# Kernel optimization log

Measured on AMD Instinct MI355X. Metric: run time of the kernel, lower is better.

## Reference

```python
import jax, jax.numpy as jnp
import numpy as np

B_, N, C = 1024, 64, 512
H = 16          # num_heads
NW = 64         # number of windows (B_ % NW == 0)


def setup_inputs() -> dict:
    key = jax.random.key(0)
    ks = jax.random.split(key, 7)
    return {
        "x": jax.random.normal(ks[0], (B_, N, C), jnp.float32),
        "mask": jax.random.normal(ks[1], (NW, N, N), jnp.float32),
        "qkv_w": jax.random.normal(ks[2], (C, 3 * C), jnp.float32) * 0.02,
        "qkv_b": jax.random.normal(ks[3], (3 * C,), jnp.float32) * 0.02,
        "proj_w": jax.random.normal(ks[4], (C, C), jnp.float32) * 0.02,
        "proj_b": jax.random.normal(ks[5], (C,), jnp.float32) * 0.02,
        "bias_table": jax.random.normal(ks[6], (2 * N - 1, H), jnp.float32) * 0.02,
    }


def reference(x, mask, qkv_w, qkv_b, proj_w, proj_b, bias_table):
    b_, n, c = x.shape
    h = bias_table.shape[1]
    ws = (bias_table.shape[0] + 1) // 2  # window_size, == n here
    d = c // h
    scale = d ** -0.5

    qkv = x @ qkv_w + qkv_b                                   # [B_, N, 3C]
    qkv = qkv.reshape(b_, n, 3, h, d).transpose(2, 0, 3, 1, 4)  # [3, B_, H, N, d]
    q, k, v = qkv[0] * scale, qkv[1], qkv[2]

    attn = jnp.einsum('bhnd,bhmd->bhnm', q, k)                # [B_, H, N, N]

    coords = jnp.arange(ws)
    rel_idx = coords[:, None] - coords[None, :] + ws - 1       # [ws, ws]
    bias = bias_table[rel_idx].transpose(2, 0, 1)              # [H, ws, ws]
    attn = attn + bias[None]

    nw = mask.shape[0]
    attn = attn.reshape(b_ // nw, nw, h, n, n) + mask[None, :, None]
    attn = attn.reshape(-1, h, n, n)
    attn = jax.nn.softmax(attn, axis=-1)

    out = jnp.einsum('bhnm,bhmd->bhnd', attn, v)               # [B_, H, N, d]
    # Faithful to the TF code: v keeps a leading singleton dim after tf.split,
    # so attn@v is [1, B_, H, N, d]; perm [0,2,1,3,4] swaps B_ and H before
    # the final reshape to (B_, N, C).
    out = out[None].transpose(0, 2, 1, 3, 4).reshape(b_, n, c)
    return out @ proj_w + proj_b
```

## Files before the change

kernel.cpp:

```cpp
#include <hip/hip_runtime.h>
#include <hip/hip_bf16.h>
#include <stdint.h>

typedef __attribute__((ext_vector_type(4))) float f32x4;
typedef __attribute__((ext_vector_type(8))) short s16x8;

__device__ __forceinline__ short f2bf(float f) {
  union { float f; uint32_t u; } v; v.f = f;
  uint32_t r = v.u + 0x7FFFu + ((v.u >> 16) & 1u);
  return (short)(r >> 16);
}
__device__ __forceinline__ uint32_t pack2bf(float a, float b) {
  return (uint32_t)(uint16_t)f2bf(a) | ((uint32_t)(uint16_t)f2bf(b) << 16);
}

__device__ __forceinline__ void async16(const void* g, void* l) {
  __builtin_amdgcn_global_load_lds(
      (const __attribute__((address_space(1))) void*)g,
      (__attribute__((address_space(3))) void*)l, 16, 0, 0);
}

__global__ __launch_bounds__(256) void k_cast_bf16(const float* __restrict__ in,
                                                   short* __restrict__ out, int n8) {
  int i = blockIdx.x * 256 + threadIdx.x;
  if (i >= n8) return;
  const float4* p = (const float4*)in + (size_t)i * 2;
  float4 a = p[0], b = p[1];
  s16x8 o;
  o[0] = f2bf(a.x); o[1] = f2bf(a.y); o[2] = f2bf(a.z); o[3] = f2bf(a.w);
  o[4] = f2bf(b.x); o[5] = f2bf(b.y); o[6] = f2bf(b.z); o[7] = f2bf(b.w);
  ((s16x8*)out)[i] = o;
}

__global__ __launch_bounds__(256) void k_transpose_cast(const float* __restrict__ in,
                                                        short* __restrict__ out,
                                                        int K, int N) {
  __shared__ float tile[64][65];
  const int bx = blockIdx.x;
  const int by = blockIdx.y;
  const int tx = threadIdx.x & 63, ty = threadIdx.x >> 6;
#pragma unroll
  for (int r = ty; r < 64; r += 4)
    tile[r][tx] = in[(size_t)(by * 64 + r) * N + bx * 64 + tx];
  __syncthreads();
#pragma unroll
  for (int r = ty; r < 64; r += 4)
    out[(size_t)(bx * 64 + r) * K + by * 64 + tx] = f2bf(tile[tx][r]);
}

#define TILE_SH 16384

template <int OUTMODE, int NBN, int KK>
__global__ __launch_bounds__(512, 2) void k_gemm256p(const short* __restrict__ A,
                                                     const short* __restrict__ Bw,
                                                     const float* __restrict__ bias,
                                                     void* __restrict__ C,
                                                     int N, int nrounds) {
  __shared__ short lds[2 * 2 * TILE_SH];
  const int t = threadIdx.x;
  const int w = t >> 6, l = t & 63;
  const int wm = w >> 2, wn = w & 3;
  const int swz = (((int)blockIdx.x & 7) << 5) + ((int)blockIdx.x >> 3);

  const int NT = KK >> 6;
  const int NS = nrounds * NT;

  auto stage = [&](const short* __restrict__ G, int row0, int kt, short* dst) {
#pragma unroll
    for (int L = 0; L < 2; ++L) {
      int cw = L * 512 + (t & ~63);
      int c = cw + l;
      int r = c >> 3, s = c & 7;
      async16(G + (size_t)(row0 + r) * KK + kt + ((s ^ (r & 7)) << 3), dst + cw * 8);
    }
  };
  auto issueA = [&](int step, int bmv, int hf) {
    int kt = step & 7;
    stage(A, bmv * 256 + hf * 128, kt * 64, lds + (kt & 1) * 32768 + hf * 8192);
  };
  auto issueB = [&](int step, int bnv, int hf) {
    int kt = step & 7;
    stage(Bw, bnv * 256 + hf * 128, kt * 64, lds + (kt & 1) * 32768 + TILE_SH + hf * 8192);
  };

  const int g = l >> 4, v = l & 7;
  int ofsA[2], ofsB[2];
#pragma unroll
  for (int ks = 0; ks < 2; ++ks) {
    ofsA[ks] = (wm * 128 + (l & 15)) * 64 + (((ks * 4 + g) ^ v) << 3);
    ofsB[ks] = (wn * 64 + (l & 15)) * 64 + (((ks * 4 + g) ^ v) << 3);
  }

  f32x4 acc[8][4] = {};
  s16x8 bfr[4][2];

  {
    const int bm0 = swz / NBN, bn0 = swz % NBN;
    issueB(0, bn0, 0); issueB(0, bn0, 1);
    issueA(0, bm0, 0); issueA(0, bm0, 1);
    issueB(1, bn0, 0); issueB(1, bn0, 1);
  }
  asm volatile("s_waitcnt vmcnt(4)" ::: "memory");
  __builtin_amdgcn_s_barrier();

#define PHASE(AI0, STAGE_STMT, TAIL_STMT)                                                                      \
  {                                                                                                            \
    s16x8 a00 = *(const s16x8*)(Ab + ofsA[0] + (AI0) * 1024);                                                  \
    s16x8 a01 = *(const s16x8*)(Ab + ofsA[1] + (AI0) * 1024);                                                  \
    s16x8 a10 = *(const s16x8*)(Ab + ofsA[0] + ((AI0) + 1) * 1024);                                            \
    s16x8 a11 = *(const s16x8*)(Ab + ofsA[1] + ((AI0) + 1) * 1024);                                            \
    STAGE_STMT;                                                                                                \
    __builtin_amdgcn_s_barrier();                                                                              \
    asm volatile("s_waitcnt lgkmcnt(0)" ::: "memory");                                                         \
    __builtin_amdgcn_s_setprio(1);                                                                             \
    _Pragma("unroll")                                                                                          \
    for (int nj = 0; nj < 4; ++nj) {                                                                           \
      acc[(AI0)][nj] = __builtin_amdgcn_mfma_f32_16x16x32_bf16(a00, bfr[nj][0], acc[(AI0)][nj], 0, 0, 0);      \
      acc[(AI0)][nj] = __builtin_amdgcn_mfma_f32_16x16x32_bf16(a01, bfr[nj][1], acc[(AI0)][nj], 0, 0, 0);      \
      acc[(AI0) + 1][nj] = __builtin_amdgcn_mfma_f32_16x16x32_bf16(a10, bfr[nj][0], acc[(AI0) + 1][nj], 0, 0, 0); \
      acc[(AI0) + 1][nj] = __builtin_amdgcn_mfma_f32_16x16x32_bf16(a11, bfr[nj][1], acc[(AI0) + 1][nj], 0, 0, 0); \
    }                                                                                                          \
    __builtin_amdgcn_s_setprio(0);                                                                             \
    TAIL_STMT;                                                                                                 \
    __builtin_amdgcn_s_barrier();                                                                              \
  }

  for (int j = 0; j < nrounds; ++j) {
    const int tauc = swz + (j << 8);
    const int bmc = tauc / NBN, bnc = tauc % NBN;
    for (int T = 0; T < NT; ++T) {
      const int s = (j << 3) + T;
      const int s1 = s + 1, s2 = s + 2;
      const int tau1 = swz + (((s1) >> 3) << 8);
      const int tau2 = swz + (((s2) >> 3) << 8);
      const int bm1 = tau1 / NBN;
      const int bn2 = tau2 % NBN;
      const short* Ab = lds + (T & 1) * 32768;
      const short* Bb = Ab + TILE_SH;
#pragma unroll
      for (int nj = 0; nj < 4; ++nj)
#pragma unroll
        for (int ks = 0; ks < 2; ++ks)
          bfr[nj][ks] = *(const s16x8*)(Bb + ofsB[ks] + nj * 1024);

      PHASE(0, if (s1 < NS) issueA(s1, bm1, 0), );
      PHASE(2, if (s1 < NS) issueA(s1, bm1, 1), );
      PHASE(4, if (s2 < NS) issueB(s2, bn2, 0), );
      PHASE(6, if (s2 < NS) issueB(s2, bn2, 1),
            if (s2 < NS) { asm volatile("s_waitcnt vmcnt(4)" ::: "memory"); }
            else if (s1 < NS) { asm volatile("s_waitcnt vmcnt(0)" ::: "memory"); });
    }

#pragma unroll
    for (int ai = 0; ai < 8; ++ai)
#pragma unroll
      for (int nj = 0; nj < 4; ++nj) {
        int col = bnc * 256 + wn * 64 + nj * 16 + (l & 15);
        float bv = bias[col];
#pragma unroll
        for (int r = 0; r < 4; ++r) {
          int row = bmc * 256 + wm * 128 + ai * 16 + (l >> 4) * 4 + r;
          float vv = acc[ai][nj][r] + bv;
          if (OUTMODE == 1) {
            ((float*)C)[(size_t)row * N + col] = vv;
          } else if (OUTMODE == 0) {
            ((short*)C)[(size_t)row * N + col] = f2bf(vv);
          } else {
            int bb = row >> 6, nn = row & 63;
            int sel = col >> 9, hh = (col >> 5) & 15, dd = col & 31;
            ((short*)C)[(((size_t)(bb * 48 + hh * 3 + sel)) << 11) + (nn << 5) + dd] = f2bf(vv);
          }
        }
      }
#pragma unroll
    for (int ai = 0; ai < 8; ++ai)
#pragma unroll
      for (int nj = 0; nj < 4; ++nj)
        acc[ai][nj] = (f32x4){0.f, 0.f, 0.f, 0.f};
  }
#undef PHASE
}

__global__ __launch_bounds__(256) void k_attn(const short* __restrict__ qkv2,
                                              const float* __restrict__ mask,
                                              const float* __restrict__ bias_table,
                                              short* __restrict__ Y) {
  __shared__ float mask_lds[64 * 64];
  __shared__ float bias_lds[4][128];
  __shared__ short p_lds[4][64][72];
  __shared__ short v_lds[4][64][40];

  const int t = threadIdx.x, wv = t >> 6, ln = t & 63;
  const int b = blockIdx.x;
  const int h = blockIdx.y * 4 + wv;
  const int hi = ln >> 4, lo = ln & 15;

  const float4* mk = (const float4*)(mask + (size_t)(b & 63) * 4096);
#pragma unroll
  for (int u = 0; u < 4; ++u) {
    int idx = t + 256 * u;
    int row = idx >> 4, c4 = (idx & 15) * 4;
    *(float4*)&mask_lds[row * 64 + (c4 ^ ((row & 7) << 2))] = mk[idx];
  }
  for (int u = ln; u < 127; u += 64) bias_lds[wv][u] = bias_table[u * 16 + h];

  const short* base = qkv2 + ((size_t)(b * 16 + h)) * 3 * 2048;
  const short* vg = base + 4096;
#pragma unroll
  for (int u = 0; u < 4; ++u) {
    int row = u * 16 + (ln >> 2), c8 = (ln & 3) * 8;
    *(s16x8*)&v_lds[wv][row][c8] = *(const s16x8*)(vg + row * 32 + c8);
  }
  __syncthreads();

  s16x8 qf[4], kf[4];
#pragma unroll
  for (int i = 0; i < 4; ++i) {
    qf[i] = *(const s16x8*)(base + (16 * i + lo) * 32 + hi * 8);
    kf[i] = *(const s16x8*)(base + 2048 + (16 * i + lo) * 32 + hi * 8);
  }
  f32x4 s2[4][4] = {};
#pragma unroll
  for (int j = 0; j < 4; ++j)
#pragma unroll
    for (int i = 0; i < 4; ++i)
      s2[j][i] = __builtin_amdgcn_mfma_f32_16x16x32_bf16(kf[j], qf[i], s2[j][i], 0, 0, 0);

  const float scale = 0.17677669529663687f;
#pragma unroll
  for (int i = 0; i < 4; ++i) {
    const int n = 16 * i + lo;
    const int msw = (n & 7) << 2;
    float x[16];
    float vmax = -1e30f;
#pragma unroll
    for (int j = 0; j < 4; ++j)
#pragma unroll
      for (int r = 0; r < 4; ++r) {
        int m = 16 * j + 4 * hi + r;
        float xx = s2[j][i][r] * scale + bias_lds[wv][n - m + 63] +
                   mask_lds[n * 64 + (m ^ msw)];
        x[j * 4 + r] = xx;
        vmax = fmaxf(vmax, xx);
      }
    vmax = fmaxf(vmax, __shfl_xor(vmax, 16, 64));
    vmax = fmaxf(vmax, __shfl_xor(vmax, 32, 64));
    float sum = 0.f;
#pragma unroll
    for (int u = 0; u < 16; ++u) {
      x[u] = __expf(x[u] - vmax);
      sum += x[u];
    }
    sum += __shfl_xor(sum, 16, 64);
    sum += __shfl_xor(sum, 32, 64);
    float rsv = 1.0f / sum;
#pragma unroll
    for (int j = 0; j < 4; ++j)
#pragma unroll
      for (int rp = 0; rp < 2; ++rp)
        *(uint32_t*)&p_lds[wv][n][16 * j + 4 * hi + rp * 2] =
            pack2bf(x[j * 4 + rp * 2] * rsv, x[j * 4 + rp * 2 + 1] * rsv);
  }

  f32x4 o2[2][4] = {};
#pragma unroll
  for (int kk = 0; kk < 2; ++kk) {
    s16x8 pa[4];
#pragma unroll
    for (int i2 = 0; i2 < 4; ++i2)
      pa[i2] = *(const s16x8*)&p_lds[wv][16 * i2 + lo][kk * 32 + hi * 8];
#pragma unroll
    for (int j2 = 0; j2 < 2; ++j2) {
      s16x8 vf;
#pragma unroll
      for (int jj = 0; jj < 8; ++jj)
        vf[jj] = v_lds[wv][kk * 32 + hi * 8 + jj][16 * j2 + lo];
#pragma unroll
      for (int i2 = 0; i2 < 4; ++i2)
        o2[j2][i2] = __builtin_amdgcn_mfma_f32_16x16x32_bf16(vf, pa[i2], o2[j2][i2], 0, 0, 0);
    }
  }

  const int rr = h * 64 + (b >> 4);
#pragma unroll
  for (int i2 = 0; i2 < 4; ++i2) {
    int ss = (b & 15) * 4 + i2;
    short* yr = Y + ((size_t)rr * 64 + ss) * 512 + lo * 32 + 4 * hi;
#pragma unroll
    for (int j2 = 0; j2 < 2; ++j2) {
      uint2 pk;
      pk.x = pack2bf(o2[j2][i2][0], o2[j2][i2][1]);
      pk.y = pack2bf(o2[j2][i2][2], o2[j2][i2][3]);
      *(uint2*)(yr + 16 * j2) = pk;
    }
  }
}

extern "C" void kernel_launch(void* const* d_in, const int* in_sizes, int n_in,
                              void* d_out, int out_size, void* d_ws, size_t ws_size,
                              hipStream_t stream) {
  const float* x      = (const float*)d_in[0];
  const float* mask   = (const float*)d_in[1];
  const float* qkv_w  = (const float*)d_in[2];
  const float* qkv_b  = (const float*)d_in[3];
  const float* proj_w = (const float*)d_in[4];
  const float* proj_b = (const float*)d_in[5];
  const float* btab   = (const float*)d_in[6];
  float* out = (float*)d_out;

  char* w = (char*)d_ws;
  short* qkv_ws = (short*)w;
  short* xbf    = (short*)(w + (size_t)65536 * 1536 * 2);
  short* Y      = xbf;
  short* wT     = (short*)(w + (size_t)65536 * 1536 * 2 + (size_t)65536 * 512 * 2);
  short* projT  = wT + 1536 * 512;

  k_cast_bf16<<<16384, 256, 0, stream>>>(x, xbf, 33554432 / 8);
  k_transpose_cast<<<dim3(24, 8), 256, 0, stream>>>(qkv_w, wT, 512, 1536);
  k_transpose_cast<<<dim3(8, 8), 256, 0, stream>>>(proj_w, projT, 512, 512);
  k_gemm256p<2, 6, 512><<<256, 512, 0, stream>>>(xbf, wT, qkv_b, qkv_ws, 1536, 6);
  k_attn<<<dim3(1024, 4), 256, 0, stream>>>(qkv_ws, mask, btab, Y);
  k_gemm256p<1, 2, 512><<<256, 512, 0, stream>>>(Y, projT, proj_b, out, 512, 2);
}
```

Baseline: 289.4 us.

## Double-buffer A fragments in registers and restage GEMM prologue

Result: slower. 395.4 us (+36.6%).

```diff
diff --git a/kernel.cpp b/kernel.cpp
--- a/kernel.cpp
+++ b/kernel.cpp
@@ -93,37 +93,42 @@
 
   f32x4 acc[8][4] = {};
   s16x8 bfr[4][2];
+  s16x8 fE[4], fO[4];
+
+#define RD_A4(D, BASE, AI0)                                        \
+  D[0] = *(const s16x8*)((BASE) + ofsA[0] + (AI0) * 1024);         \
+  D[1] = *(const s16x8*)((BASE) + ofsA[1] + (AI0) * 1024);         \
+  D[2] = *(const s16x8*)((BASE) + ofsA[0] + ((AI0) + 1) * 1024);   \
+  D[3] = *(const s16x8*)((BASE) + ofsA[1] + ((AI0) + 1) * 1024);
+
+#define RD_B8(BASE)                                                \
+  _Pragma("unroll")                                                \
+  for (int nj = 0; nj < 4; ++nj) {                                 \
+    bfr[nj][0] = *(const s16x8*)((BASE) + ofsB[0] + nj * 1024);    \
+    bfr[nj][1] = *(const s16x8*)((BASE) + ofsB[1] + nj * 1024);    \
+  }
+
+#define MFMA16(D, AI0)                                                                                          \
+  __builtin_amdgcn_s_setprio(1);                                                                                \
+  _Pragma("unroll")                                                                                             \
+  for (int nj = 0; nj < 4; ++nj) {                                                                              \
+    acc[(AI0)][nj] = __builtin_amdgcn_mfma_f32_16x16x32_bf16(D[0], bfr[nj][0], acc[(AI0)][nj], 0, 0, 0);        \
+    acc[(AI0)][nj] = __builtin_amdgcn_mfma_f32_16x16x32_bf16(D[1], bfr[nj][1], acc[(AI0)][nj], 0, 0, 0);        \
+    acc[(AI0) + 1][nj] = __builtin_amdgcn_mfma_f32_16x16x32_bf16(D[2], bfr[nj][0], acc[(AI0) + 1][nj], 0, 0, 0); \
+    acc[(AI0) + 1][nj] = __builtin_amdgcn_mfma_f32_16x16x32_bf16(D[3], bfr[nj][1], acc[(AI0) + 1][nj], 0, 0, 0); \
+  }                                                                                                             \
+  __builtin_amdgcn_s_setprio(0);
 
   {
     const int bm0 = swz / NBN, bn0 = swz % NBN;
+    issueA(0, bm0, 0); issueA(0, bm0, 1);
     issueB(0, bn0, 0); issueB(0, bn0, 1);
-    issueA(0, bm0, 0); issueA(0, bm0, 1);
+    issueA(1, bm0, 0); issueA(1, bm0, 1);
     issueB(1, bn0, 0); issueB(1, bn0, 1);
   }
-  asm volatile("s_waitcnt vmcnt(4)" ::: "memory");
+  asm volatile("s_waitcnt vmcnt(8)" ::: "memory");
   __builtin_amdgcn_s_barrier();
-
-#define PHASE(AI0, STAGE_STMT, TAIL_STMT)                                                                      \
-  {                                                                                                            \
-    s16x8 a00 = *(const s16x8*)(Ab + ofsA[0] + (AI0) * 1024);                                                  \
-    s16x8 a01 = *(const s16x8*)(Ab + ofsA[1] + (AI0) * 1024);                                                  \
-    s16x8 a10 = *(const s16x8*)(Ab + ofsA[0] + ((AI0) + 1) * 1024);                                            \
-    s16x8 a11 = *(const s16x8*)(Ab + ofsA[1] + ((AI0) + 1) * 1024);                                            \
-    STAGE_STMT;                                                                                                \
-    __builtin_amdgcn_s_barrier();                                                                              \
-    asm volatile("s_waitcnt lgkmcnt(0)" ::: "memory");                                                         \
-    __builtin_amdgcn_s_setprio(1);                                                                             \
-    _Pragma("unroll")                                                                                          \
-    for (int nj = 0; nj < 4; ++nj) {                                                                           \
-      acc[(AI0)][nj] = __builtin_amdgcn_mfma_f32_16x16x32_bf16(a00, bfr[nj][0], acc[(AI0)][nj], 0, 0, 0);      \
-      acc[(AI0)][nj] = __builtin_amdgcn_mfma_f32_16x16x32_bf16(a01, bfr[nj][1], acc[(AI0)][nj], 0, 0, 0);      \
-      acc[(AI0) + 1][nj] = __builtin_amdgcn_mfma_f32_16x16x32_bf16(a10, bfr[nj][0], acc[(AI0) + 1][nj], 0, 0, 0); \
-      acc[(AI0) + 1][nj] = __builtin_amdgcn_mfma_f32_16x16x32_bf16(a11, bfr[nj][1], acc[(AI0) + 1][nj], 0, 0, 0); \
-    }                                                                                                          \
-    __builtin_amdgcn_s_setprio(0);                                                                             \
-    TAIL_STMT;                                                                                                 \
-    __builtin_amdgcn_s_barrier();                                                                              \
-  }
+  RD_A4(fE, lds, 0);
 
   for (int j = 0; j < nrounds; ++j) {
     const int tauc = swz + (j << 8);
@@ -131,24 +136,39 @@
     for (int T = 0; T < NT; ++T) {
       const int s = (j << 3) + T;
       const int s1 = s + 1, s2 = s + 2;
-      const int tau1 = swz + (((s1) >> 3) << 8);
-      const int tau2 = swz + (((s2) >> 3) << 8);
+      const int tau1 = swz + ((s1 >> 3) << 8);
+      const int tau2 = swz + ((s2 >> 3) << 8);
       const int bm1 = tau1 / NBN;
       const int bn2 = tau2 % NBN;
       const short* Ab = lds + (T & 1) * 32768;
       const short* Bb = Ab + TILE_SH;
-#pragma unroll
-      for (int nj = 0; nj < 4; ++nj)
-#pragma unroll
-        for (int ks = 0; ks < 2; ++ks)
-          bfr[nj][ks] = *(const s16x8*)(Bb + ofsB[ks] + nj * 1024);
-
-      PHASE(0, if (s1 < NS) issueA(s1, bm1, 0), );
-      PHASE(2, if (s1 < NS) issueA(s1, bm1, 1), );
-      PHASE(4, if (s2 < NS) issueB(s2, bn2, 0), );
-      PHASE(6, if (s2 < NS) issueB(s2, bn2, 1),
-            if (s2 < NS) { asm volatile("s_waitcnt vmcnt(4)" ::: "memory"); }
-            else if (s1 < NS) { asm volatile("s_waitcnt vmcnt(0)" ::: "memory"); });
+      const short* Ab1 = lds + ((T + 1) & 1) * 32768;
+
+      RD_B8(Bb);
+      RD_A4(fO, Ab, 2);
+      if (s > 0 && s1 < NS) issueA(s1, bm1, 0);
+      __builtin_amdgcn_s_barrier();
+      MFMA16(fE, 0);
+
+      RD_A4(fE, Ab, 4);
+      if (s > 0 && s1 < NS) issueA(s1, bm1, 1);
+      __builtin_amdgcn_s_barrier();
+      MFMA16(fO, 2);
+
+      RD_A4(fO, Ab, 6);
+      if (s2 < NS) {
+        issueB(s2, bn2, 0);
+        asm volatile("s_waitcnt vmcnt(2)" ::: "memory");
+      } else if (s1 < NS) {
+        asm volatile("s_waitcnt vmcnt(0)" ::: "memory");
+      }
+      __builtin_amdgcn_s_barrier();
+      MFMA16(fE, 4);
+
+      if (s1 < NS) { RD_A4(fE, Ab1, 0); }
+      if (s2 < NS) issueB(s2, bn2, 1);
+      __builtin_amdgcn_s_barrier();
+      MFMA16(fO, 6);
     }
 
 #pragma unroll
@@ -178,7 +198,9 @@
       for (int nj = 0; nj < 4; ++nj)
         acc[ai][nj] = (f32x4){0.f, 0.f, 0.f, 0.f};
   }
-#undef PHASE
+#undef RD_A4
+#undef RD_B8
+#undef MFMA16
 }
 
 __global__ __launch_bounds__(256) void k_attn(const short* __restrict__ qkv2,
```

## Fuse x cast, QKV projection and window attention into one kernel

Applied to the files above, without the earlier changes.

Result: slower. 334.1 us (+15.4%).

```diff
diff --git a/kernel.cpp b/kernel.cpp
--- a/kernel.cpp
+++ b/kernel.cpp
@@ -18,18 +18,6 @@
   __builtin_amdgcn_global_load_lds(
       (const __attribute__((address_space(1))) void*)g,
       (__attribute__((address_space(3))) void*)l, 16, 0, 0);
-}
-
-__global__ __launch_bounds__(256) void k_cast_bf16(const float* __restrict__ in,
-                                                   short* __restrict__ out, int n8) {
-  int i = blockIdx.x * 256 + threadIdx.x;
-  if (i >= n8) return;
-  const float4* p = (const float4*)in + (size_t)i * 2;
-  float4 a = p[0], b = p[1];
-  s16x8 o;
-  o[0] = f2bf(a.x); o[1] = f2bf(a.y); o[2] = f2bf(a.z); o[3] = f2bf(a.w);
-  o[4] = f2bf(b.x); o[5] = f2bf(b.y); o[6] = f2bf(b.z); o[7] = f2bf(b.w);
-  ((s16x8*)out)[i] = o;
 }
 
 __global__ __launch_bounds__(256) void k_transpose_cast(const float* __restrict__ in,
@@ -46,6 +34,209 @@
 #pragma unroll
   for (int r = ty; r < 64; r += 4)
     out[(size_t)(bx * 64 + r) * K + by * 64 + tx] = f2bf(tile[tx][r]);
+}
+
+__global__ __launch_bounds__(256, 1) void k_fused(const float* __restrict__ x,
+                                                  const short* __restrict__ wT,
+                                                  const float* __restrict__ qkvb,
+                                                  const float* __restrict__ mask,
+                                                  const float* __restrict__ btab,
+                                                  short* __restrict__ Y) {
+  __shared__ __align__(16) short x_lds[64 * 512];
+  __shared__ __align__(16) float mask_lds[64 * 64];
+  __shared__ float bias_all[16][128];
+  __shared__ float qb_lds[1536];
+  __shared__ __align__(16) short qk_lds[4][2][64][40];
+  __shared__ __align__(16) short v_lds[4][64][40];
+
+  const int t = threadIdx.x, wv = t >> 6, ln = t & 63;
+  const int w = blockIdx.x;
+  const int hi = ln >> 4, lo = ln & 15;
+
+  const float* xw = x + (size_t)w * 32768;
+#pragma unroll
+  for (int u = 0; u < 16; ++u) {
+    int c = u * 256 + t;
+    int row = c >> 6, cs = c & 63;
+    const float* src = xw + row * 512 + cs * 8;
+    float4 f0 = *(const float4*)src;
+    float4 f1 = *(const float4*)(src + 4);
+    s16x8 o;
+    o[0] = f2bf(f0.x); o[1] = f2bf(f0.y); o[2] = f2bf(f0.z); o[3] = f2bf(f0.w);
+    o[4] = f2bf(f1.x); o[5] = f2bf(f1.y); o[6] = f2bf(f1.z); o[7] = f2bf(f1.w);
+    *(s16x8*)&x_lds[row * 512 + ((cs ^ (row & 7)) << 3)] = o;
+  }
+  const float4* mk = (const float4*)(mask + (size_t)(w & 63) * 4096);
+#pragma unroll
+  for (int u = 0; u < 4; ++u) {
+    int idx = t + 256 * u;
+    int row = idx >> 4, c4 = (idx & 15) * 4;
+    *(float4*)&mask_lds[row * 64 + (c4 ^ ((row & 7) << 2))] = mk[idx];
+  }
+#pragma unroll
+  for (int u = 0; u < 8; ++u) {
+    int idx = t + 256 * u;
+    if (idx < 2032) bias_all[idx & 15][idx >> 4] = btab[idx];
+  }
+#pragma unroll
+  for (int u = 0; u < 6; ++u) qb_lds[t + 256 * u] = qkvb[t + 256 * u];
+  __syncthreads();
+
+  short* q0 = &qk_lds[wv][0][0][0];
+  short* k0 = &qk_lds[wv][1][0][0];
+  short* vv = &v_lds[wv][0][0];
+  short* P  = q0;
+
+  const float scale = 0.17677669529663687f;
+  const int rr_base = (w >> 4);
+
+  for (int hh = 0; hh < 4; ++hh) {
+    const int h = wv * 4 + hh;
+
+    const short* wbase[6];
+#pragma unroll
+    for (int f = 0; f < 6; ++f) {
+      int sel = f >> 1, njj = f & 1;
+      wbase[f] = wT + (size_t)(sel * 512 + h * 32 + njj * 16 + lo) * 512 + hi * 8;
+    }
+    f32x4 acc[4][6] = {};
+    s16x8 wfA[6], wfB[6];
+#pragma unroll
+    for (int f = 0; f < 6; ++f) wfA[f] = *(const s16x8*)(wbase[f]);
+
+#pragma unroll
+    for (int kt2 = 0; kt2 < 8; ++kt2) {
+      {
+        const int kt = 2 * kt2;
+#pragma unroll
+        for (int f = 0; f < 6; ++f) wfB[f] = *(const s16x8*)(wbase[f] + (kt + 1) * 32);
+        s16x8 xf[4];
+#pragma unroll
+        for (int mi = 0; mi < 4; ++mi)
+          xf[mi] = *(const s16x8*)&x_lds[(16 * mi + lo) * 512 + (((kt * 4 + hi) ^ (lo & 7)) << 3)];
+#pragma unroll
+        for (int mi = 0; mi < 4; ++mi)
+#pragma unroll
+          for (int f = 0; f < 6; ++f)
+            acc[mi][f] = __builtin_amdgcn_mfma_f32_16x16x32_bf16(wfA[f], xf[mi], acc[mi][f], 0, 0, 0);
+      }
+      {
+        const int kt = 2 * kt2 + 1;
+        if (kt2 < 7) {
+#pragma unroll
+          for (int f = 0; f < 6; ++f) wfA[f] = *(const s16x8*)(wbase[f] + (kt + 1) * 32);
+        }
+        s16x8 xf[4];
+#pragma unroll
+        for (int mi = 0; mi < 4; ++mi)
+          xf[mi] = *(const s16x8*)&x_lds[(16 * mi + lo) * 512 + (((kt * 4 + hi) ^ (lo & 7)) << 3)];
+#pragma unroll
+        for (int mi = 0; mi < 4; ++mi)
+#pragma unroll
+          for (int f = 0; f < 6; ++f)
+            acc[mi][f] = __builtin_amdgcn_mfma_f32_16x16x32_bf16(wfB[f], xf[mi], acc[mi][f], 0, 0, 0);
+      }
+    }
+
+#pragma unroll
+    for (int f = 0; f < 6; ++f) {
+      int sel = f >> 1, njj = f & 1;
+      float4 b4 = *(const float4*)&qb_lds[sel * 512 + h * 32 + njj * 16 + 4 * hi];
+      short* dst = (sel == 0) ? q0 : (sel == 1) ? k0 : vv;
+#pragma unroll
+      for (int mi = 0; mi < 4; ++mi) {
+        float v0 = acc[mi][f][0] + b4.x, v1 = acc[mi][f][1] + b4.y;
+        float v2 = acc[mi][f][2] + b4.z, v3 = acc[mi][f][3] + b4.w;
+        if (sel == 0) { v0 *= scale; v1 *= scale; v2 *= scale; v3 *= scale; }
+        uint2 pk;
+        pk.x = pack2bf(v0, v1);
+        pk.y = pack2bf(v2, v3);
+        *(uint2*)&dst[(16 * mi + lo) * 40 + njj * 16 + 4 * hi] = pk;
+      }
+    }
+    asm volatile("s_waitcnt lgkmcnt(0)" ::: "memory");
+
+    s16x8 qf[4], kf[4];
+#pragma unroll
+    for (int i = 0; i < 4; ++i) {
+      qf[i] = *(const s16x8*)&q0[(16 * i + lo) * 40 + hi * 8];
+      kf[i] = *(const s16x8*)&k0[(16 * i + lo) * 40 + hi * 8];
+    }
+    f32x4 s2[4][4] = {};
+#pragma unroll
+    for (int j = 0; j < 4; ++j)
+#pragma unroll
+      for (int i = 0; i < 4; ++i)
+        s2[j][i] = __builtin_amdgcn_mfma_f32_16x16x32_bf16(kf[j], qf[i], s2[j][i], 0, 0, 0);
+
+#pragma unroll
+    for (int i = 0; i < 4; ++i) {
+      const int n = 16 * i + lo;
+      const int msw = (n & 7) << 2;
+      float xv[16];
+      float vmax = -1e30f;
+#pragma unroll
+      for (int j = 0; j < 4; ++j)
+#pragma unroll
+        for (int r = 0; r < 4; ++r) {
+          int m = 16 * j + 4 * hi + r;
+          float xx = s2[j][i][r] + bias_all[h][n - m + 63] + mask_lds[n * 64 + (m ^ msw)];
+          xv[j * 4 + r] = xx;
+          vmax = fmaxf(vmax, xx);
+        }
+      vmax = fmaxf(vmax, __shfl_xor(vmax, 16, 64));
+      vmax = fmaxf(vmax, __shfl_xor(vmax, 32, 64));
+      float sum = 0.f;
+#pragma unroll
+      for (int u = 0; u < 16; ++u) {
+        xv[u] = __expf(xv[u] - vmax);
+        sum += xv[u];
+      }
+      sum += __shfl_xor(sum, 16, 64);
+      sum += __shfl_xor(sum, 32, 64);
+      float rsv = 1.0f / sum;
+#pragma unroll
+      for (int j = 0; j < 4; ++j)
+#pragma unroll
+        for (int rp = 0; rp < 2; ++rp)
+          *(uint32_t*)&P[n * 72 + 16 * j + 4 * hi + rp * 2] =
+              pack2bf(xv[j * 4 + rp * 2] * rsv, xv[j * 4 + rp * 2 + 1] * rsv);
+    }
+    asm volatile("s_waitcnt lgkmcnt(0)" ::: "memory");
+
+    f32x4 o2[2][4] = {};
+#pragma unroll
+    for (int kk = 0; kk < 2; ++kk) {
+      s16x8 pa[4];
+#pragma unroll
+      for (int i2 = 0; i2 < 4; ++i2)
+        pa[i2] = *(const s16x8*)&P[(16 * i2 + lo) * 72 + kk * 32 + hi * 8];
+#pragma unroll
+      for (int j2 = 0; j2 < 2; ++j2) {
+        s16x8 vf;
+#pragma unroll
+        for (int jj = 0; jj < 8; ++jj)
+          vf[jj] = vv[(kk * 32 + hi * 8 + jj) * 40 + 16 * j2 + lo];
+#pragma unroll
+        for (int i2 = 0; i2 < 4; ++i2)
+          o2[j2][i2] = __builtin_amdgcn_mfma_f32_16x16x32_bf16(vf, pa[i2], o2[j2][i2], 0, 0, 0);
+      }
+    }
+
+    const int rr = h * 64 + rr_base;
+#pragma unroll
+    for (int i2 = 0; i2 < 4; ++i2) {
+      int ss = (w & 15) * 4 + i2;
+      short* yr = Y + ((size_t)rr * 64 + ss) * 512 + lo * 32 + 4 * hi;
+#pragma unroll
+      for (int j2 = 0; j2 < 2; ++j2) {
+        uint2 pk;
+        pk.x = pack2bf(o2[j2][i2][0], o2[j2][i2][1]);
+        pk.y = pack2bf(o2[j2][i2][2], o2[j2][i2][3]);
+        *(uint2*)(yr + 16 * j2) = pk;
+      }
+    }
+  }
 }
 
 #define TILE_SH 16384
@@ -131,8 +322,8 @@
     for (int T = 0; T < NT; ++T) {
       const int s = (j << 3) + T;
       const int s1 = s + 1, s2 = s + 2;
-      const int tau1 = swz + (((s1) >> 3) << 8);
-      const int tau2 = swz + (((s2) >> 3) << 8);
+      const int tau1 = swz + ((s1 >> 3) << 8);
+      const int tau2 = swz + ((s2 >> 3) << 8);
       const int bm1 = tau1 / NBN;
       const int bn2 = tau2 % NBN;
       const short* Ab = lds + (T & 1) * 32768;
@@ -163,12 +354,8 @@
           float vv = acc[ai][nj][r] + bv;
           if (OUTMODE == 1) {
             ((float*)C)[(size_t)row * N + col] = vv;
-          } else if (OUTMODE == 0) {
+          } else {
             ((short*)C)[(size_t)row * N + col] = f2bf(vv);
-          } else {
-            int bb = row >> 6, nn = row & 63;
-            int sel = col >> 9, hh = (col >> 5) & 15, dd = col & 31;
-            ((short*)C)[(((size_t)(bb * 48 + hh * 3 + sel)) << 11) + (nn << 5) + dd] = f2bf(vv);
           }
         }
       }
@@ -179,121 +366,6 @@
         acc[ai][nj] = (f32x4){0.f, 0.f, 0.f, 0.f};
   }
 #undef PHASE
-}
-
-__global__ __launch_bounds__(256) void k_attn(const short* __restrict__ qkv2,
-                                              const float* __restrict__ mask,
-                                              const float* __restrict__ bias_table,
-                                              short* __restrict__ Y) {
-  __shared__ float mask_lds[64 * 64];
-  __shared__ float bias_lds[4][128];
-  __shared__ short p_lds[4][64][72];
-  __shared__ short v_lds[4][64][40];
-
-  const int t = threadIdx.x, wv = t >> 6, ln = t & 63;
-  const int b = blockIdx.x;
-  const int h = blockIdx.y * 4 + wv;
-  const int hi = ln >> 4, lo = ln & 15;
-
-  const float4* mk = (const float4*)(mask + (size_t)(b & 63) * 4096);
-#pragma unroll
-  for (int u = 0; u < 4; ++u) {
-    int idx = t + 256 * u;
-    int row = idx >> 4, c4 = (idx & 15) * 4;
-    *(float4*)&mask_lds[row * 64 + (c4 ^ ((row & 7) << 2))] = mk[idx];
-  }
-  for (int u = ln; u < 127; u += 64) bias_lds[wv][u] = bias_table[u * 16 + h];
-
-  const short* base = qkv2 + ((size_t)(b * 16 + h)) * 3 * 2048;
-  const short* vg = base + 4096;
-#pragma unroll
-  for (int u = 0; u < 4; ++u) {
-    int row = u * 16 + (ln >> 2), c8 = (ln & 3) * 8;
-    *(s16x8*)&v_lds[wv][row][c8] = *(const s16x8*)(vg + row * 32 + c8);
-  }
-  __syncthreads();
-
-  s16x8 qf[4], kf[4];
-#pragma unroll
-  for (int i = 0; i < 4; ++i) {
-    qf[i] = *(const s16x8*)(base + (16 * i + lo) * 32 + hi * 8);
-    kf[i] = *(const s16x8*)(base + 2048 + (16 * i + lo) * 32 + hi * 8);
-  }
-  f32x4 s2[4][4] = {};
-#pragma unroll
-  for (int j = 0; j < 4; ++j)
-#pragma unroll
-    for (int i = 0; i < 4; ++i)
-      s2[j][i] = __builtin_amdgcn_mfma_f32_16x16x32_bf16(kf[j], qf[i], s2[j][i], 0, 0, 0);
-
-  const float scale = 0.17677669529663687f;
-#pragma unroll
-  for (int i = 0; i < 4; ++i) {
-    const int n = 16 * i + lo;
-    const int msw = (n & 7) << 2;
-    float x[16];
-    float vmax = -1e30f;
-#pragma unroll
-    for (int j = 0; j < 4; ++j)
-#pragma unroll
-      for (int r = 0; r < 4; ++r) {
-        int m = 16 * j + 4 * hi + r;
-        float xx = s2[j][i][r] * scale + bias_lds[wv][n - m + 63] +
-                   mask_lds[n * 64 + (m ^ msw)];
-        x[j * 4 + r] = xx;
-        vmax = fmaxf(vmax, xx);
-      }
-    vmax = fmaxf(vmax, __shfl_xor(vmax, 16, 64));
-    vmax = fmaxf(vmax, __shfl_xor(vmax, 32, 64));
-    float sum = 0.f;
-#pragma unroll
-    for (int u = 0; u < 16; ++u) {
-      x[u] = __expf(x[u] - vmax);
-      sum += x[u];
-    }
-    sum += __shfl_xor(sum, 16, 64);
-    sum += __shfl_xor(sum, 32, 64);
-    float rsv = 1.0f / sum;
-#pragma unroll
-    for (int j = 0; j < 4; ++j)
-#pragma unroll
-      for (int rp = 0; rp < 2; ++rp)
-        *(uint32_t*)&p_lds[wv][n][16 * j + 4 * hi + rp * 2] =
-            pack2bf(x[j * 4 + rp * 2] * rsv, x[j * 4 + rp * 2 + 1] * rsv);
-  }
-
-  f32x4 o2[2][4] = {};
-#pragma unroll
-  for (int kk = 0; kk < 2; ++kk) {
-    s16x8 pa[4];
-#pragma unroll
-    for (int i2 = 0; i2 < 4; ++i2)
-      pa[i2] = *(const s16x8*)&p_lds[wv][16 * i2 + lo][kk * 32 + hi * 8];
-#pragma unroll
-    for (int j2 = 0; j2 < 2; ++j2) {
-      s16x8 vf;
-#pragma unroll
-      for (int jj = 0; jj < 8; ++jj)
-        vf[jj] = v_lds[wv][kk * 32 + hi * 8 + jj][16 * j2 + lo];
-#pragma unroll
-      for (int i2 = 0; i2 < 4; ++i2)
-        o2[j2][i2] = __builtin_amdgcn_mfma_f32_16x16x32_bf16(vf, pa[i2], o2[j2][i2], 0, 0, 0);
-    }
-  }
-
-  const int rr = h * 64 + (b >> 4);
-#pragma unroll
-  for (int i2 = 0; i2 < 4; ++i2) {
-    int ss = (b & 15) * 4 + i2;
-    short* yr = Y + ((size_t)rr * 64 + ss) * 512 + lo * 32 + 4 * hi;
-#pragma unroll
-    for (int j2 = 0; j2 < 2; ++j2) {
-      uint2 pk;
-      pk.x = pack2bf(o2[j2][i2][0], o2[j2][i2][1]);
-      pk.y = pack2bf(o2[j2][i2][2], o2[j2][i2][3]);
-      *(uint2*)(yr + 16 * j2) = pk;
-    }
-  }
 }
 
 extern "C" void kernel_launch(void* const* d_in, const int* in_sizes, int n_in,
@@ -309,16 +381,12 @@
   float* out = (float*)d_out;
 
   char* w = (char*)d_ws;
-  short* qkv_ws = (short*)w;
-  short* xbf    = (short*)(w + (size_t)65536 * 1536 * 2);
-  short* Y      = xbf;
-  short* wT     = (short*)(w + (size_t)65536 * 1536 * 2 + (size_t)65536 * 512 * 2);
-  short* projT  = wT + 1536 * 512;
-
-  k_cast_bf16<<<16384, 256, 0, stream>>>(x, xbf, 33554432 / 8);
+  short* Y     = (short*)w;
+  short* wT    = (short*)(w + (size_t)65536 * 512 * 2);
+  short* projT = wT + 1536 * 512;
+
   k_transpose_cast<<<dim3(24, 8), 256, 0, stream>>>(qkv_w, wT, 512, 1536);
   k_transpose_cast<<<dim3(8, 8), 256, 0, stream>>>(proj_w, projT, 512, 512);
-  k_gemm256p<2, 6, 512><<<256, 512, 0, stream>>>(xbf, wT, qkv_b, qkv_ws, 1536, 6);
-  k_attn<<<dim3(1024, 4), 256, 0, stream>>>(qkv_ws, mask, btab, Y);
+  k_fused<<<1024, 256, 0, stream>>>(x, wT, qkv_b, mask, btab, Y);
   k_gemm256p<1, 2, 512><<<256, 512, 0, stream>>>(Y, projT, proj_b, out, 512, 2);
 }
```
